# Optimization experiments

Hardware: AMD Instinct MI355X
Metric: run time of the kernel (lower is better)

Reference implementation:

```python
import jax, jax.numpy as jnp
import numpy as np
from jax import lax

B, L, D_MODEL = 8, 4096, 256
EXPAND, D_STATE, D_CONV = 4, 16, 4
D_INNER = EXPAND * D_MODEL          # 1024
DT_RANK = (D_MODEL + 15) // 16      # 16
EPS = 1e-5


def setup_inputs() -> dict:
    key = jax.random.key(0)
    ks = jax.random.split(key, 12)

    def w(k, shape, fan_in):
        return jax.random.normal(k, shape, jnp.float32) / np.sqrt(fan_in)

    # realistic dt bias: inverse-softplus of dt ~ LogUniform(1e-3, 0.1)
    dt0 = jnp.exp(jax.random.uniform(ks[10], (D_INNER,), jnp.float32)
                  * (np.log(0.1) - np.log(1e-3)) + np.log(1e-3))
    return {
        "x": jax.random.normal(ks[0], (B, L, D_MODEL), jnp.float32),
        "norm_w": jnp.ones((D_MODEL,), jnp.float32),
        "in_proj_w": w(ks[1], (2 * D_INNER, D_MODEL), D_MODEL),
        "conv_w": w(ks[2], (D_INNER, 1, D_CONV), D_CONV),   # depthwise causal conv
        "conv_b": jnp.zeros((D_INNER,), jnp.float32),
        "x_proj_w": w(ks[3], (DT_RANK + 2 * D_STATE, D_INNER), D_INNER),
        "dt_proj_w": w(ks[4], (D_INNER, DT_RANK), DT_RANK),
        "dt_proj_b": jnp.log(jnp.expm1(dt0)),
        "A_log": jnp.log(jnp.tile(jnp.arange(1, D_STATE + 1, dtype=jnp.float32), (D_INNER, 1))),
        "D": jnp.ones((D_INNER,), jnp.float32),
        "out_proj_w": w(ks[5], (D_MODEL, D_INNER), D_INNER),
    }


def _selective_scan(dt, Bm, Cm, x, A):
    # dt, x: [B,L,d_inner]; Bm, Cm: [B,L,d_state]; A: [d_inner,d_state]
    def step(h, inp):
        dt_t, B_t, C_t, x_t = inp                         # [B,d], [B,n], [B,n], [B,d]
        dA = jnp.exp(dt_t[..., None] * A)                 # [B,d,n] in (0,1)
        dBx = (dt_t * x_t)[..., None] * B_t[:, None, :]   # [B,d,n]
        h = dA * h + dBx
        y = jnp.einsum('bdn,bn->bd', h, C_t)
        return h, y

    h0 = jnp.zeros((dt.shape[0], A.shape[0], A.shape[1]), dt.dtype)
    xs = (dt.swapaxes(0, 1), Bm.swapaxes(0, 1), Cm.swapaxes(0, 1), x.swapaxes(0, 1))
    _, ys = lax.scan(step, h0, xs)                        # ys: [L,B,d]
    return ys.swapaxes(0, 1)


def reference(x, norm_w, in_proj_w, conv_w, conv_b, x_proj_w,
              dt_proj_w, dt_proj_b, A_log, D, out_proj_w):
    # Block (fused_add_norm=False), n_layer=1: residual=x; h=RMSNorm(residual)
    residual = x
    h = residual * lax.rsqrt(jnp.mean(residual * residual, -1, keepdims=True) + EPS) * norm_w

    # Mamba mixer
    xz = jnp.einsum('bld,ed->ble', h, in_proj_w)          # [B,L,2*d_inner]
    xc, z = jnp.split(xz, 2, axis=-1)

    # depthwise causal conv1d over L, then SiLU
    xc_t = xc.swapaxes(1, 2)                              # [B,d_inner,L]
    xconv = lax.conv_general_dilated(
        xc_t, conv_w, (1,), [(D_CONV - 1, 0)],
        dimension_numbers=('NCH', 'OIH', 'NCH'),
        feature_group_count=D_INNER) + conv_b[None, :, None]
    xa = jax.nn.silu(xconv).swapaxes(1, 2)                # [B,L,d_inner]

    # input-dependent dt, B, C
    x_dbl = jnp.einsum('bld,ed->ble', xa, x_proj_w)
    dt, Bm, Cm = jnp.split(x_dbl, [DT_RANK, DT_RANK + D_STATE], axis=-1)
    dt = jax.nn.softplus(jnp.einsum('blr,dr->bld', dt, dt_proj_w) + dt_proj_b)

    A = -jnp.exp(A_log)                                   # [d_inner,d_state], negative
    y = _selective_scan(dt, Bm, Cm, xa, A)
    y = (y + xa * D) * jax.nn.silu(z)                     # skip term + gate
    out = jnp.einsum('bld,ed->ble', y, out_proj_w)        # [B,L,d_model]

    # MambaBlock epilogue: forward_f + for_residual
    return out + residual
```

## Files before the change

kernel.cpp:

```cpp
#include <hip/hip_runtime.h>
#include <hip/hip_bf16.h>
#include <cstdint>
#include <cstddef>

typedef __bf16 bf16;
typedef __attribute__((ext_vector_type(8))) __bf16 bf16x8;
typedef __attribute__((ext_vector_type(2))) __bf16 bf16x2;
typedef __attribute__((ext_vector_type(4))) float f32x4;

#define BB 8
#define LL 4096
#define DMODEL 256
#define DINNER 1024
#define MT (BB*LL)
#define CT 8
#define DTMCH 64

__constant__ float LOGT[16] = {
    0.0f, 0.6931471806f, 1.0986122887f, 1.3862943611f,
    1.6094379124f, 1.7917594692f, 1.9459101091f, 2.0794415417f,
    2.1972245773f, 2.3025850930f, 2.3978952728f, 2.4849066498f,
    2.5649493575f, 2.6390573296f, 2.7080502011f, 2.7725887222f};

__global__ __launch_bounds__(256) void k_wsfail(float* out, int n){
    int i = blockIdx.x*256 + threadIdx.x;
    if (i < n) out[i] = 1e9f;
}

__global__ __launch_bounds__(256) void k_cast3(const float* __restrict__ s1, const float* __restrict__ s2,
                                               const float* __restrict__ s3,
                                               bf16* __restrict__ o1, bf16* __restrict__ o2, bf16* __restrict__ o3,
                                               int n1, int n2, int n3){
    int i = blockIdx.x*256 + threadIdx.x;
    if (i < n1) o1[i] = (bf16)s1[i];
    else if (i < n1+n2) o2[i-n1] = (bf16)s2[i-n1];
    else if (i < n1+n2+n3) o3[i-n1-n2] = (bf16)s3[i-n1-n2];
}

__global__ __launch_bounds__(256) void k_rms(const float* __restrict__ x, const float* __restrict__ w,
                                             bf16* __restrict__ h){
    int m = blockIdx.x, t = threadIdx.x;
    float v = x[(size_t)m*DMODEL + t];
    float s = v*v;
    #pragma unroll
    for (int o=1;o<64;o<<=1) s += __shfl_xor(s, o, 64);
    __shared__ float ps[4];
    if ((t&63)==0) ps[t>>6] = s;
    __syncthreads();
    float tot = ps[0]+ps[1]+ps[2]+ps[3];
    float inv = rsqrtf(tot*(1.0f/DMODEL) + 1e-5f);
    h[(size_t)m*DMODEL + t] = (bf16)(v*inv*w[t]);
}

template<int MODE, bool NMASK>
__global__ __launch_bounds__(256) void k_gemm(const bf16* __restrict__ A, const bf16* __restrict__ Bw,
                                              bf16* __restrict__ C1, bf16* __restrict__ C2,
                                              float* __restrict__ Cf, const float* __restrict__ res,
                                              int M, int N, int K){
    __shared__ __align__(16) bf16 As[128][40];
    __shared__ __align__(16) bf16 Bs[128][40];
    const int tid  = threadIdx.x;
    const int m0   = blockIdx.x*128, n0 = blockIdx.y*128;
    const int wave = tid>>6, lane = tid&63;
    const int wr   = wave>>1, wc = wave&1;
    const int fr   = lane&15, kg = lane>>4;
    const int srow = tid>>1, shalf = tid&1;

    f32x4 acc[4][4] = {};

    for (int kt=0; kt<K; kt+=32){
        {
            const bf16* g = A + (size_t)(m0+srow)*K + kt + shalf*16;
            uint4 v0 = *(const uint4*)g;
            uint4 v1 = *(const uint4*)(g+8);
            *(uint4*)&As[srow][shalf*16]   = v0;
            *(uint4*)&As[srow][shalf*16+8] = v1;
        }
        {
            uint4 v0 = make_uint4(0,0,0,0), v1 = make_uint4(0,0,0,0);
            int nr = n0 + srow;
            if (!NMASK || nr < N){
                const bf16* g = Bw + (size_t)nr*K + kt + shalf*16;
                v0 = *(const uint4*)g; v1 = *(const uint4*)(g+8);
            }
            *(uint4*)&Bs[srow][shalf*16]   = v0;
            *(uint4*)&Bs[srow][shalf*16+8] = v1;
        }
        __syncthreads();
        bf16x8 af[4], bfv[4];
        #pragma unroll
        for (int i=0;i<4;i++) af[i]  = *(const bf16x8*)&As[wr*64 + i*16 + fr][kg*8];
        #pragma unroll
        for (int j=0;j<4;j++) bfv[j] = *(const bf16x8*)&Bs[wc*64 + j*16 + fr][kg*8];
        #pragma unroll
        for (int i=0;i<4;i++)
            #pragma unroll
            for (int j=0;j<4;j++)
                acc[i][j] = __builtin_amdgcn_mfma_f32_16x16x32_bf16(af[i], bfv[j], acc[i][j], 0,0,0);
        __syncthreads();
    }
    #pragma unroll
    for (int i=0;i<4;i++)
        #pragma unroll
        for (int j=0;j<4;j++)
            #pragma unroll
            for (int r=0;r<4;r++){
                int row = m0 + wr*64 + i*16 + kg*4 + r;
                int col = n0 + wc*64 + j*16 + fr;
                float v = acc[i][j][r];
                if (MODE==0){
                    if (!NMASK || col < N) C1[(size_t)row*N + col] = (bf16)v;
                } else if (MODE==1){
                    bf16* dst = (col < 1024) ? C1 : C2;
                    dst[(size_t)row*1024 + (col & 1023)] = (bf16)v;
                } else {
                    size_t o = (size_t)row*N + col;
                    Cf[o] = v + res[o];
                }
            }
}

__global__ __launch_bounds__(256) void k_conv(const bf16* __restrict__ xc, const float* __restrict__ cw,
                                              const float* __restrict__ cb, bf16* __restrict__ xa){
    int i  = blockIdx.x*256 + threadIdx.x;
    int dv = i & 127;
    int mc = i >> 7;
    int d0 = dv*8;
    int m0 = mc*CT;
    int t0 = m0 & (LL-1);

    float4 w4[8];
    #pragma unroll
    for (int q=0;q<8;q++) w4[q] = *(const float4*)(cw + (size_t)(d0+q)*4);
    float bias[8];
    {
        float4 b0 = *(const float4*)(cb + d0);
        float4 b1 = *(const float4*)(cb + d0 + 4);
        bias[0]=b0.x; bias[1]=b0.y; bias[2]=b0.z; bias[3]=b0.w;
        bias[4]=b1.x; bias[5]=b1.y; bias[6]=b1.z; bias[7]=b1.w;
    }
    const bf16* base = xc + (size_t)m0*DINNER + d0;
    bf16* outp       = xa + (size_t)m0*DINNER + d0;
    bf16x8 p3 = {}, p2 = {}, p1 = {};
    if (t0 > 0){
        p3 = *(const bf16x8*)(base - 3*DINNER);
        p2 = *(const bf16x8*)(base - 2*DINNER);
        p1 = *(const bf16x8*)(base - 1*DINNER);
    }
    #pragma unroll
    for (int s=0;s<CT;s++){
        bf16x8 cur = *(const bf16x8*)(base + (size_t)s*DINNER);
        bf16x8 o;
        #pragma unroll
        for (int q=0;q<8;q++){
            float a = bias[q];
            a = fmaf((float)p3[q],  w4[q].x, a);
            a = fmaf((float)p2[q],  w4[q].y, a);
            a = fmaf((float)p1[q],  w4[q].z, a);
            a = fmaf((float)cur[q], w4[q].w, a);
            o[q] = (bf16)(a/(1.f+__expf(-a)));
        }
        *(bf16x8*)(outp + (size_t)s*DINNER) = o;
        p3 = p2; p2 = p1; p1 = cur;
    }
}

__device__ __forceinline__ float softplus_f(float a){
    return fmaxf(a, 0.f) + __logf(1.f + __expf(-fabsf(a)));
}

__device__ __forceinline__ void powchain(float p, float* pw){
    pw[0]=p;
    pw[1]=pw[0]*pw[0];  pw[2]=pw[1]*pw[0];  pw[3]=pw[1]*pw[1];
    pw[4]=pw[1]*pw[2];  pw[5]=pw[2]*pw[2];  pw[6]=pw[2]*pw[3];  pw[7]=pw[3]*pw[3];
    pw[8]=pw[3]*pw[4];  pw[9]=pw[4]*pw[4];  pw[10]=pw[4]*pw[5]; pw[11]=pw[5]*pw[5];
    pw[12]=pw[5]*pw[6]; pw[13]=pw[6]*pw[6]; pw[14]=pw[6]*pw[7]; pw[15]=pw[7]*pw[7];
}

__global__ __launch_bounds__(256) void k_dt(const bf16* __restrict__ xdbl, const float* __restrict__ dtw,
                                            const float* __restrict__ dtb, bf16* __restrict__ dty){
    int d     = (blockIdx.x & 3)*256 + threadIdx.x;
    int mbase = (blockIdx.x >> 2)*DTMCH;
    float4 w[4];
    #pragma unroll
    for (int q=0;q<4;q++) w[q] = ((const float4*)(dtw + (size_t)d*16))[q];
    float bias = dtb[d];
    __shared__ __align__(16) bf16 xs[DTMCH][16];
    if (threadIdx.x < DTMCH*2){
        int r = threadIdx.x>>1, half = threadIdx.x&1;
        *(uint4*)&xs[r][half*8] = *(const uint4*)(xdbl + (size_t)(mbase+r)*48 + half*8);
    }
    __syncthreads();
    for (int s=0;s<DTMCH;s++){
        bf16x8 x0 = *(const bf16x8*)&xs[s][0];
        bf16x8 x1 = *(const bf16x8*)&xs[s][8];
        float a = bias;
        a=fmaf((float)x0[0],w[0].x,a); a=fmaf((float)x0[1],w[0].y,a);
        a=fmaf((float)x0[2],w[0].z,a); a=fmaf((float)x0[3],w[0].w,a);
        a=fmaf((float)x0[4],w[1].x,a); a=fmaf((float)x0[5],w[1].y,a);
        a=fmaf((float)x0[6],w[1].z,a); a=fmaf((float)x0[7],w[1].w,a);
        a=fmaf((float)x1[0],w[2].x,a); a=fmaf((float)x1[1],w[2].y,a);
        a=fmaf((float)x1[2],w[2].z,a); a=fmaf((float)x1[3],w[2].w,a);
        a=fmaf((float)x1[4],w[3].x,a); a=fmaf((float)x1[5],w[3].y,a);
        a=fmaf((float)x1[6],w[3].z,a); a=fmaf((float)x1[7],w[3].w,a);
        dty[(size_t)(mbase+s)*DINNER + d] = (bf16)softplus_f(a);
    }
}

template<int LCHT>
__global__ __launch_bounds__(256) void k_pass1(const bf16* __restrict__ dty, const bf16* __restrict__ xa,
                                               const bf16* __restrict__ xdbl, const float* __restrict__ Alog,
                                               bf16* __restrict__ Sp, float* __restrict__ Tp, int nch){
    int tid = threadIdx.x;
    int d0  = (blockIdx.x*256 + tid)*2;
    int c = blockIdx.y, b = blockIdx.z;
    int mbase = b*LL + c*LCHT;

    __shared__ __align__(16) float Bs[LCHT][16];
    for (int idx=tid; idx<LCHT*2; idx+=256){
        int row = idx>>1, part = idx&1;
        bf16x8 v = *(const bf16x8*)(xdbl + (size_t)(mbase+row)*48 + 16 + part*8);
        #pragma unroll
        for (int q=0;q<8;q++) Bs[row][part*8+q] = (float)v[q];
    }
    bool st = true;
    float Al0[16], Al1[16];
    {
        const float4* Ap = (const float4*)(Alog + (size_t)d0*16);
        #pragma unroll
        for (int q=0;q<4;q++){
            float4 a4 = Ap[q];   Al0[q*4]=a4.x; Al0[q*4+1]=a4.y; Al0[q*4+2]=a4.z; Al0[q*4+3]=a4.w;
            float4 b4 = Ap[4+q]; Al1[q*4]=b4.x; Al1[q*4+1]=b4.y; Al1[q*4+2]=b4.z; Al1[q*4+3]=b4.w;
        }
        #pragma unroll
        for (int n=0;n<16;n++) st = st && (fabsf(Al0[n]-LOGT[n])<1e-4f) && (fabsf(Al1[n]-LOGT[n])<1e-4f);
    }
    __syncthreads();

    float S0[16], S1[16];
    #pragma unroll
    for (int n=0;n<16;n++){ S0[n]=0.f; S1[n]=0.f; }
    float sdt0 = 0.f, sdt1 = 0.f;

    if (st){
        const bf16* dp = dty + (size_t)mbase*DINNER + d0;
        const bf16* xp = xa  + (size_t)mbase*DINNER + d0;
        bf16x2 cdt[4], cxa[4], ndt[4], nxa[4];
        #pragma unroll
        for (int g2=0;g2<4;g2++){
            cdt[g2] = *(const bf16x2*)(dp + (size_t)g2*DINNER);
            cxa[g2] = *(const bf16x2*)(xp + (size_t)g2*DINNER);
        }
        size_t off = 0;
        for (int s0=0; s0<LCHT; s0+=4){
            size_t poff = (s0+4 < LCHT) ? off + 4*DINNER : off;
            #pragma unroll
            for (int g2=0;g2<4;g2++){
                ndt[g2] = *(const bf16x2*)(dp + poff + (size_t)g2*DINNER);
                nxa[g2] = *(const bf16x2*)(xp + poff + (size_t)g2*DINNER);
            }
            #pragma unroll
            for (int g2=0;g2<4;g2++){
                int s = s0 + g2;
                float dt0=(float)cdt[g2][0], dt1=(float)cdt[g2][1];
                float dx0=dt0*(float)cxa[g2][0], dx1=dt1*(float)cxa[g2][1];
                float pw0[16], pw1[16];
                powchain(__expf(-dt0), pw0);
                powchain(__expf(-dt1), pw1);
                #pragma unroll
                for (int q=0;q<4;q++){
                    float4 b4 = *(const float4*)&Bs[s][q*4];
                    S0[q*4+0]=fmaf(pw0[q*4+0],S0[q*4+0],dx0*b4.x); S1[q*4+0]=fmaf(pw1[q*4+0],S1[q*4+0],dx1*b4.x);
                    S0[q*4+1]=fmaf(pw0[q*4+1],S0[q*4+1],dx0*b4.y); S1[q*4+1]=fmaf(pw1[q*4+1],S1[q*4+1],dx1*b4.y);
                    S0[q*4+2]=fmaf(pw0[q*4+2],S0[q*4+2],dx0*b4.z); S1[q*4+2]=fmaf(pw1[q*4+2],S1[q*4+2],dx1*b4.z);
                    S0[q*4+3]=fmaf(pw0[q*4+3],S0[q*4+3],dx0*b4.w); S1[q*4+3]=fmaf(pw1[q*4+3],S1[q*4+3],dx1*b4.w);
                }
                sdt0 += dt0; sdt1 += dt1;
            }
            #pragma unroll
            for (int g2=0;g2<4;g2++){ cdt[g2]=ndt[g2]; cxa[g2]=nxa[g2]; }
            off = poff;
        }
    } else {
        float An0[16], An1[16];
        #pragma unroll
        for (int n=0;n<16;n++){ An0[n] = -__expf(Al0[n]); An1[n] = -__expf(Al1[n]); }
        for (int s=0;s<LCHT;s++){
            size_t off = (size_t)(mbase+s)*DINNER + d0;
            bf16x2 pdt = *(const bf16x2*)(dty+off);
            bf16x2 pxa = *(const bf16x2*)(xa +off);
            float dt0=(float)pdt[0], dt1=(float)pdt[1];
            float dx0=dt0*(float)pxa[0], dx1=dt1*(float)pxa[1];
            #pragma unroll
            for (int n=0;n<16;n++){
                S0[n] = fmaf(__expf(dt0*An0[n]), S0[n], dx0*Bs[s][n]);
                S1[n] = fmaf(__expf(dt1*An1[n]), S1[n], dx1*Bs[s][n]);
            }
            sdt0 += dt0; sdt1 += dt1;
        }
    }
    size_t cb   = (size_t)(b*nch + c);
    size_t base = (cb*DINNER + d0)*16;
    bf16x8 o0, o1, o2, o3;
    #pragma unroll
    for (int q=0;q<8;q++){
        o0[q] = (bf16)S0[q];   o1[q] = (bf16)S0[8+q];
        o2[q] = (bf16)S1[q];   o3[q] = (bf16)S1[8+q];
    }
    *(bf16x8*)&Sp[base]    = o0;
    *(bf16x8*)&Sp[base+8]  = o1;
    *(bf16x8*)&Sp[base+16] = o2;
    *(bf16x8*)&Sp[base+24] = o3;
    *(float2*)&Tp[cb*DINNER + d0] = make_float2(sdt0, sdt1);
}

__global__ __launch_bounds__(256) void k_pass2(bf16* __restrict__ Sp, const float* __restrict__ Tp,
                                               const float* __restrict__ Alog, int nch){
    int i = blockIdx.x*256 + threadIdx.x;
    int b   = i >> 13;
    int low = (i & 8191)*2;
    int d   = low >> 4;
    int n0  = low & 15;
    float An0 = -__expf(Alog[d*16+n0]);
    float An1 = -__expf(Alog[d*16+n0+1]);
    float2 h = make_float2(0.f, 0.f);
    for (int c=0;c<nch;c++){
        size_t cb = (size_t)(b*nch + c);
        float sdt = Tp[cb*DINNER + d];
        size_t idx = cb*16384 + low;
        bf16x2 Sv = *(const bf16x2*)&Sp[idx];
        float P0 = __expf(An0*sdt);
        float P1 = __expf(An1*sdt);
        bf16x2 hw;
        hw[0] = (bf16)h.x; hw[1] = (bf16)h.y;
        *(bf16x2*)&Sp[idx] = hw;
        h.x = fmaf(P0, h.x, (float)Sv[0]);
        h.y = fmaf(P1, h.y, (float)Sv[1]);
    }
}

template<int LCHT>
__global__ __launch_bounds__(256) void k_pass3(bf16* __restrict__ dty, const bf16* __restrict__ xa,
                                               const bf16* __restrict__ xdbl, const bf16* __restrict__ z,
                                               const float* __restrict__ Alog, const float* __restrict__ Dp,
                                               const bf16* __restrict__ Sp, int nch){
    int tid = threadIdx.x;
    int d0  = (blockIdx.x*256 + tid)*2;
    int c = blockIdx.y, b = blockIdx.z;
    int mbase = b*LL + c*LCHT;

    __shared__ __align__(16) float BCs[LCHT][32];
    for (int idx=tid; idx<LCHT*4; idx+=256){
        int row = idx>>2, part = idx&3;
        bf16x8 v = *(const bf16x8*)(xdbl + (size_t)(mbase+row)*48 + 16 + part*8);
        #pragma unroll
        for (int q=0;q<8;q++) BCs[row][part*8+q] = (float)v[q];
    }
    bool st = true;
    float Al0[16], Al1[16];
    {
        const float4* Ap = (const float4*)(Alog + (size_t)d0*16);
        #pragma unroll
        for (int q=0;q<4;q++){
            float4 a4 = Ap[q];   Al0[q*4]=a4.x; Al0[q*4+1]=a4.y; Al0[q*4+2]=a4.z; Al0[q*4+3]=a4.w;
            float4 b4 = Ap[4+q]; Al1[q*4]=b4.x; Al1[q*4+1]=b4.y; Al1[q*4+2]=b4.z; Al1[q*4+3]=b4.w;
        }
        #pragma unroll
        for (int n=0;n<16;n++) st = st && (fabsf(Al0[n]-LOGT[n])<1e-4f) && (fabsf(Al1[n]-LOGT[n])<1e-4f);
    }
    float h0[16], h1[16];
    {
        size_t hbase = ((size_t)(b*nch + c)*DINNER + d0)*16;
        bf16x8 a8 = *(const bf16x8*)&Sp[hbase];
        bf16x8 b8 = *(const bf16x8*)&Sp[hbase+8];
        bf16x8 c8 = *(const bf16x8*)&Sp[hbase+16];
        bf16x8 d8 = *(const bf16x8*)&Sp[hbase+24];
        #pragma unroll
        for (int q=0;q<8;q++){
            h0[q]   = (float)a8[q];  h0[8+q] = (float)b8[q];
            h1[q]   = (float)c8[q];  h1[8+q] = (float)d8[q];
        }
    }
    float Dd0 = Dp[d0], Dd1 = Dp[d0+1];
    __syncthreads();

    if (st){
        bf16*       dp = dty + (size_t)mbase*DINNER + d0;
        const bf16* xp = xa  + (size_t)mbase*DINNER + d0;
        const bf16* zp = z   + (size_t)mbase*DINNER + d0;
        bf16x2 cdt[4], cxa[4], cz[4], ndt[4], nxa[4], nz[4];
        #pragma unroll
        for (int g2=0;g2<4;g2++){
            cdt[g2] = *(const bf16x2*)(dp + (size_t)g2*DINNER);
            cxa[g2] = *(const bf16x2*)(xp + (size_t)g2*DINNER);
            cz[g2]  = *(const bf16x2*)(zp + (size_t)g2*DINNER);
        }
        size_t off = 0;
        for (int s0=0; s0<LCHT; s0+=4){
            size_t poff = (s0+4 < LCHT) ? off + 4*DINNER : off;
            #pragma unroll
            for (int g2=0;g2<4;g2++){
                ndt[g2] = *(const bf16x2*)(dp + poff + (size_t)g2*DINNER);
                nxa[g2] = *(const bf16x2*)(xp + poff + (size_t)g2*DINNER);
                nz[g2]  = *(const bf16x2*)(zp + poff + (size_t)g2*DINNER);
            }
            #pragma unroll
            for (int g2=0;g2<4;g2++){
                int s = s0 + g2;
                float dt0=(float)cdt[g2][0], dt1=(float)cdt[g2][1];
                float xv0=(float)cxa[g2][0], xv1=(float)cxa[g2][1];
                float dx0=dt0*xv0, dx1=dt1*xv1;
                float pw0[16], pw1[16];
                powchain(__expf(-dt0), pw0);
                powchain(__expf(-dt1), pw1);
                float yv0 = 0.f, yv1 = 0.f;
                #pragma unroll
                for (int q=0;q<4;q++){
                    float4 b4 = *(const float4*)&BCs[s][q*4];
                    float4 c4 = *(const float4*)&BCs[s][16+q*4];
                    h0[q*4+0]=fmaf(pw0[q*4+0],h0[q*4+0],dx0*b4.x); yv0=fmaf(h0[q*4+0],c4.x,yv0);
                    h1[q*4+0]=fmaf(pw1[q*4+0],h1[q*4+0],dx1*b4.x); yv1=fmaf(h1[q*4+0],c4.x,yv1);
                    h0[q*4+1]=fmaf(pw0[q*4+1],h0[q*4+1],dx0*b4.y); yv0=fmaf(h0[q*4+1],c4.y,yv0);
                    h1[q*4+1]=fmaf(pw1[q*4+1],h1[q*4+1],dx1*b4.y); yv1=fmaf(h1[q*4+1],c4.y,yv1);
                    h0[q*4+2]=fmaf(pw0[q*4+2],h0[q*4+2],dx0*b4.z); yv0=fmaf(h0[q*4+2],c4.z,yv0);
                    h1[q*4+2]=fmaf(pw1[q*4+2],h1[q*4+2],dx1*b4.z); yv1=fmaf(h1[q*4+2],c4.z,yv1);
                    h0[q*4+3]=fmaf(pw0[q*4+3],h0[q*4+3],dx0*b4.w); yv0=fmaf(h0[q*4+3],c4.w,yv0);
                    h1[q*4+3]=fmaf(pw1[q*4+3],h1[q*4+3],dx1*b4.w); yv1=fmaf(h1[q*4+3],c4.w,yv1);
                }
                float zv0=(float)cz[g2][0], zv1=(float)cz[g2][1];
                float g0 = zv0/(1.f+__expf(-zv0));
                float g1 = zv1/(1.f+__expf(-zv1));
                bf16x2 yo;
                yo[0] = (bf16)((yv0 + xv0*Dd0)*g0);
                yo[1] = (bf16)((yv1 + xv1*Dd1)*g1);
                *(bf16x2*)(dp + off + (size_t)g2*DINNER) = yo;
            }
            #pragma unroll
            for (int g2=0;g2<4;g2++){ cdt[g2]=ndt[g2]; cxa[g2]=nxa[g2]; cz[g2]=nz[g2]; }
            off = poff;
        }
    } else {
        float An0[16], An1[16];
        #pragma unroll
        for (int n=0;n<16;n++){ An0[n] = -__expf(Al0[n]); An1[n] = -__expf(Al1[n]); }
        for (int s=0;s<LCHT;s++){
            size_t off = (size_t)(mbase+s)*DINNER + d0;
            bf16x2 pdt = *(const bf16x2*)(dty+off);
            bf16x2 pxa = *(const bf16x2*)(xa +off);
            bf16x2 pz  = *(const bf16x2*)(z  +off);
            float dt0=(float)pdt[0], dt1=(float)pdt[1];
            float xv0=(float)pxa[0], xv1=(float)pxa[1];
            float dx0=dt0*xv0, dx1=dt1*xv1;
            float yv0 = 0.f, yv1 = 0.f;
            #pragma unroll
            for (int n=0;n<16;n++){
                h0[n] = fmaf(__expf(dt0*An0[n]), h0[n], dx0*BCs[s][n]);
                yv0   = fmaf(h0[n], BCs[s][16+n], yv0);
                h1[n] = fmaf(__expf(dt1*An1[n]), h1[n], dx1*BCs[s][n]);
                yv1   = fmaf(h1[n], BCs[s][16+n], yv1);
            }
            float zv0=(float)pz[0], zv1=(float)pz[1];
            float g0 = zv0/(1.f+__expf(-zv0));
            float g1 = zv1/(1.f+__expf(-zv1));
            bf16x2 yo;
            yo[0] = (bf16)((yv0 + xv0*Dd0)*g0);
            yo[1] = (bf16)((yv1 + xv1*Dd1)*g1);
            *(bf16x2*)(dty+off) = yo;
        }
    }
}

extern "C" void kernel_launch(void* const* d_in, const int* in_sizes, int n_in,
                              void* d_out, int out_size, void* d_ws, size_t ws_size,
                              hipStream_t stream) {
    const float* x     = (const float*)d_in[0];
    const float* normw = (const float*)d_in[1];
    const float* w_in  = (const float*)d_in[2];
    const float* convw = (const float*)d_in[3];
    const float* convb = (const float*)d_in[4];
    const float* w_xp  = (const float*)d_in[5];
    const float* dtw   = (const float*)d_in[6];
    const float* dtb   = (const float*)d_in[7];
    const float* Alog  = (const float*)d_in[8];
    const float* Dp    = (const float*)d_in[9];
    const float* w_out = (const float*)d_in[10];

    const size_t WB    = ((size_t)2048*256 + 48*1024 + 256*1024)*2;
    const size_t WB_AL = (WB + 255) & ~(size_t)255;
    auto need = [WB_AL](int nb, int nch)->size_t{
        size_t rows = (size_t)nb*LL;
        size_t big  = rows*DINNER*2;
        size_t xd   = ((rows*48*2) + 255) & ~(size_t)255;
        size_t sS   = (size_t)nb*nch*DINNER*16*2;
        size_t sT   = (size_t)nb*nch*DINNER*4;
        return WB_AL + 3*big + xd + sS + sT;
    };
    const int cands[8][2] = {{8,128},{8,64},{4,256},{4,128},{4,64},{2,256},{2,128},{1,256}};
    int NB = 0, NCHv = 0;
    for (int k=0;k<8;k++) if (need(cands[k][0], cands[k][1]) <= ws_size){ NB=cands[k][0]; NCHv=cands[k][1]; break; }
    if (!NB){
        k_wsfail<<<(out_size+255)/256, 256, 0, stream>>>((float*)d_out, out_size);
        return;
    }
    const int LCHv = LL/NCHv;

    char* ws = (char*)d_ws;
    bf16* win_b  = (bf16*)ws;
    bf16* wxp_b  = (bf16*)(ws + (size_t)2048*256*2);
    bf16* wout_b = (bf16*)(ws + (size_t)2048*256*2 + (size_t)48*1024*2);

    size_t rows  = (size_t)NB*LL;
    size_t big   = rows*DINNER*2;
    size_t xd_al = ((rows*48*2) + 255) & ~(size_t)255;
    char*  ar    = ws + WB_AL;
    bf16*  xcy   = (bf16*)ar;
    bf16*  zb    = (bf16*)(ar + big);
    bf16*  xab   = (bf16*)(ar + 2*big);
    bf16*  xdb   = (bf16*)(ar + 3*big);
    bf16*  Sp    = (bf16*)(ar + 3*big + xd_al);
    float* Tp    = (float*)(Sp + (size_t)NB*NCHv*DINNER*16);
    bf16*  hb    = Sp;

    k_cast3<<<(2048*256 + 48*1024 + 256*1024)/256, 256, 0, stream>>>(
        w_in, w_xp, w_out, win_b, wxp_b, wout_b, 2048*256, 48*1024, 256*1024);

    for (int b0=0; b0<BB; b0+=NB){
        const float* xb = x + (size_t)b0*LL*DMODEL;
        float*       ob = (float*)d_out + (size_t)b0*LL*DMODEL;
        k_rms<<<(int)rows, 256, 0, stream>>>(xb, normw, hb);
        k_gemm<1,false><<<dim3((int)rows/128, 16), 256, 0, stream>>>(
            hb, win_b, xcy, zb, nullptr, nullptr, (int)rows, 2048, 256);
        k_conv<<<(int)(rows/(CT*2)), 256, 0, stream>>>(xcy, convw, convb, xab);
        k_gemm<0,true><<<dim3((int)rows/128, 1), 256, 0, stream>>>(
            xab, wxp_b, xdb, nullptr, nullptr, nullptr, (int)rows, 48, 1024);
        k_dt<<<(int)(rows/DTMCH)*4, 256, 0, stream>>>(xdb, dtw, dtb, xcy);
        if (LCHv == 64){
            k_pass1<64><<<dim3(2, NCHv, NB), 256, 0, stream>>>(xcy, xab, xdb, Alog, Sp, Tp, NCHv);
            k_pass2<<<NB*32, 256, 0, stream>>>(Sp, Tp, Alog, NCHv);
            k_pass3<64><<<dim3(2, NCHv, NB), 256, 0, stream>>>(xcy, xab, xdb, zb, Alog, Dp, Sp, NCHv);
        } else if (LCHv == 32){
            k_pass1<32><<<dim3(2, NCHv, NB), 256, 0, stream>>>(xcy, xab, xdb, Alog, Sp, Tp, NCHv);
            k_pass2<<<NB*32, 256, 0, stream>>>(Sp, Tp, Alog, NCHv);
            k_pass3<32><<<dim3(2, NCHv, NB), 256, 0, stream>>>(xcy, xab, xdb, zb, Alog, Dp, Sp, NCHv);
        } else {
            k_pass1<16><<<dim3(2, NCHv, NB), 256, 0, stream>>>(xcy, xab, xdb, Alog, Sp, Tp, NCHv);
            k_pass2<<<NB*32, 256, 0, stream>>>(Sp, Tp, Alog, NCHv);
            k_pass3<16><<<dim3(2, NCHv, NB), 256, 0, stream>>>(xcy, xab, xdb, zb, Alog, Dp, Sp, NCHv);
        }
        k_gemm<2,false><<<dim3((int)rows/128, 2), 256, 0, stream>>>(
            xcy, wout_b, nullptr, nullptr, ob, xb, (int)rows, 256, 1024);
    }
}
```

Baseline: 392.9 us.

## Stage bf16 GEMM epilogue through shared memory and retune scan chunk candidates

The bf16-output GEMM modes now write their accumulators into a padded shared-memory tile and then emit coalesced 16-byte row stores, replacing scattered 2-byte stores. The shared buffer is reused from the A/B staging tiles, which adds a barrier and more LDS for those modes. The scan chunk-count candidates change so the default picks 64 chunks (64-step chunks) per batch, and the fallback template branch now instantiates 128-step chunks. This means fewer chunks and less state traffic in the pass kernels, but less parallelism.

```diff
diff --git a/kernel.cpp b/kernel.cpp
--- a/kernel.cpp
+++ b/kernel.cpp
@@ -57,8 +57,11 @@
                                               bf16* __restrict__ C1, bf16* __restrict__ C2,
                                               float* __restrict__ Cf, const float* __restrict__ res,
                                               int M, int N, int K){
-    __shared__ __align__(16) bf16 As[128][40];
-    __shared__ __align__(16) bf16 Bs[128][40];
+    constexpr int SMEMB = (MODE==2) ? (2*128*40*2) : (128*136*2 > 2*128*40*2 ? 128*136*2 : 2*128*40*2);
+    __shared__ __align__(16) char smem[SMEMB];
+    bf16 (*As)[40] = (bf16 (*)[40])smem;
+    bf16 (*Bs)[40] = (bf16 (*)[40])(smem + 128*40*2);
+
     const int tid  = threadIdx.x;
     const int m0   = blockIdx.x*128, n0 = blockIdx.y*128;
     const int wave = tid>>6, lane = tid&63;
@@ -99,25 +102,43 @@
                 acc[i][j] = __builtin_amdgcn_mfma_f32_16x16x32_bf16(af[i], bfv[j], acc[i][j], 0,0,0);
         __syncthreads();
     }
-    #pragma unroll
-    for (int i=0;i<4;i++)
-        #pragma unroll
-        for (int j=0;j<4;j++)
-            #pragma unroll
-            for (int r=0;r<4;r++){
-                int row = m0 + wr*64 + i*16 + kg*4 + r;
-                int col = n0 + wc*64 + j*16 + fr;
-                float v = acc[i][j][r];
-                if (MODE==0){
-                    if (!NMASK || col < N) C1[(size_t)row*N + col] = (bf16)v;
-                } else if (MODE==1){
-                    bf16* dst = (col < 1024) ? C1 : C2;
-                    dst[(size_t)row*1024 + (col & 1023)] = (bf16)v;
-                } else {
+
+    if (MODE==2){
+        #pragma unroll
+        for (int i=0;i<4;i++)
+            #pragma unroll
+            for (int j=0;j<4;j++)
+                #pragma unroll
+                for (int r=0;r<4;r++){
+                    int row = m0 + wr*64 + i*16 + kg*4 + r;
+                    int col = n0 + wc*64 + j*16 + fr;
                     size_t o = (size_t)row*N + col;
-                    Cf[o] = v + res[o];
+                    Cf[o] = acc[i][j][r] + res[o];
                 }
-            }
+    } else {
+        bf16 (*Cs)[136] = (bf16 (*)[136])smem;
+        #pragma unroll
+        for (int i=0;i<4;i++)
+            #pragma unroll
+            for (int j=0;j<4;j++)
+                #pragma unroll
+                for (int r=0;r<4;r++)
+                    Cs[wr*64 + i*16 + kg*4 + r][wc*64 + j*16 + fr] = (bf16)acc[i][j][r];
+        __syncthreads();
+        int r16 = tid >> 4, l16 = tid & 15;
+        int col = l16*8;
+        bf16* dst = (MODE==0) ? C1 : ((n0 < 1024) ? C1 : C2);
+        int   ncol = (MODE==0) ? N : 1024;
+        int   nb   = (MODE==0) ? n0 : (n0 & 1023);
+        #pragma unroll
+        for (int it=0; it<8; ++it){
+            int row = r16 + it*16;
+            if (!NMASK || (n0 + col) < N){
+                bf16x8 v = *(const bf16x8*)&Cs[row][col];
+                *(bf16x8*)(dst + (size_t)(m0+row)*ncol + nb + col) = v;
+            }
+        }
+    }
 }
 
 __global__ __launch_bounds__(256) void k_conv(const bf16* __restrict__ xc, const float* __restrict__ cw,
@@ -495,7 +516,7 @@
         size_t sT   = (size_t)nb*nch*DINNER*4;
         return WB_AL + 3*big + xd + sS + sT;
     };
-    const int cands[8][2] = {{8,128},{8,64},{4,256},{4,128},{4,64},{2,256},{2,128},{1,256}};
+    const int cands[8][2] = {{8,64},{4,128},{4,64},{2,128},{2,64},{1,128},{1,64},{1,32}};
     int NB = 0, NCHv = 0;
     for (int k=0;k<8;k++) if (need(cands[k][0], cands[k][1]) <= ws_size){ NB=cands[k][0]; NCHv=cands[k][1]; break; }
     if (!NB){
@@ -543,9 +564,9 @@
             k_pass2<<<NB*32, 256, 0, stream>>>(Sp, Tp, Alog, NCHv);
             k_pass3<32><<<dim3(2, NCHv, NB), 256, 0, stream>>>(xcy, xab, xdb, zb, Alog, Dp, Sp, NCHv);
         } else {
-            k_pass1<16><<<dim3(2, NCHv, NB), 256, 0, stream>>>(xcy, xab, xdb, Alog, Sp, Tp, NCHv);
+            k_pass1<128><<<dim3(2, NCHv, NB), 256, 0, stream>>>(xcy, xab, xdb, Alog, Sp, Tp, NCHv);
             k_pass2<<<NB*32, 256, 0, stream>>>(Sp, Tp, Alog, NCHv);
-            k_pass3<16><<<dim3(2, NCHv, NB), 256, 0, stream>>>(xcy, xab, xdb, zb, Alog, Dp, Sp, NCHv);
+            k_pass3<128><<<dim3(2, NCHv, NB), 256, 0, stream>>>(xcy, xab, xdb, zb, Alog, Dp, Sp, NCHv);
         }
         k_gemm<2,false><<<dim3((int)rows/128, 2), 256, 0, stream>>>(
             xcy, wout_b, nullptr, nullptr, ob, xb, (int)rows, 256, 1024);
```

Result: faster. 364.6 us (median of 3 runs) (-7.2%).
